# Kernel optimization log

Measured on AMD Instinct MI355X. Metric: run time of the kernel, lower is better.

Reference implementation:

```python
import jax, jax.numpy as jnp
import numpy as np

EPS = 1e-5  # torch BatchNorm2d default eps

def _bn_train(x, g, b):
    # BatchNorm2d in training mode: batch statistics over (N, H, W), biased variance
    m = x.mean(axis=(0, 2, 3), keepdims=True)
    v = x.var(axis=(0, 2, 3), keepdims=True)
    return g[None, :, None, None] * (x - m) / jnp.sqrt(v + EPS) + b[None, :, None, None]

def _conv3(x, w, b):
    y = jax.lax.conv_general_dilated(x, w, (1, 1), 'SAME',
                                     dimension_numbers=('NCHW', 'OIHW', 'NCHW'))
    return y + b[None, :, None, None]

def _conv1(x, w, b):
    # 1x1 conv == per-pixel matmul; w: [out, in]
    return jnp.einsum('bchw,oc->bohw', x, w) + b[None, :, None, None]

def _projector(x, w1, b1, g1, be1, w2, b2, g2, be2):
    h = jax.nn.relu(_bn_train(_conv3(x, w1, b1), g1, be1))
    return _bn_train(_conv1(h, w2, b2), g2, be2)

def _cross_teacher_attention(s, teachers, wq, bq, wk, bk, wv, bv):
    B, C, H, W = s.shape
    scale = C ** -0.5
    q = _conv1(s, wq, bq).reshape(B, C, H * W).transpose(0, 2, 1)  # [B, HW, C]
    outs, ws = [], []
    for t in teachers:  # small fixed list of teachers (structural branch)
        k = _conv1(t, wk, bk).reshape(B, C, H * W).transpose(0, 2, 1)
        v = _conv1(t, wv, bv).reshape(B, C, H * W).transpose(0, 2, 1)
        a = jax.nn.softmax(jnp.einsum('bqc,bkc->bqk', q, k) * scale, axis=-1)  # [B, HW, HW]
        outs.append(jnp.einsum('bqk,bkc->bqc', a, v))                          # [B, HW, C]
        ws.append(a.mean(axis=-1))                                             # [B, HW]
    w = jax.nn.softmax(jnp.stack(ws, axis=-1), axis=-1)          # [B, HW, T]
    fused = jnp.einsum('bqt,tbqc->bqc', w, jnp.stack(outs, 0))   # weighted sum over teachers
    fused = fused.reshape(B, H, W, C).transpose(0, 3, 1, 2)      # [B, C, H, W]
    return s + fused

def setup_inputs() -> dict:
    key = jax.random.key(0)
    ks = jax.random.split(key, 16)
    B, C, H, W = 8, 128, 56, 56
    T = 256  # teacher projector output dim
    d = {}
    d['student_mid'] = jax.random.normal(ks[0], (B, C, H, W), jnp.float32)
    d['t1_mid'] = jax.random.normal(ks[1], (B, C, H, W), jnp.float32)
    d['t2_mid'] = jax.random.normal(ks[2], (B, C, H, W), jnp.float32)
    for i, n in enumerate(['q', 'k', 'v']):
        d['w' + n] = jax.random.normal(ks[3 + i], (C, C), jnp.float32) * 0.05
        d['b' + n] = jnp.zeros((C,), jnp.float32)
    for p, off in (('p1', 6), ('p2', 10)):
        d[p + '_w1'] = jax.random.normal(ks[off], (C, C, 3, 3), jnp.float32) * 0.05
        d[p + '_b1'] = jnp.zeros((C,), jnp.float32)
        d[p + '_g1'] = jnp.ones((C,), jnp.float32)
        d[p + '_be1'] = jnp.zeros((C,), jnp.float32)
        d[p + '_w2'] = jax.random.normal(ks[off + 1], (T, C), jnp.float32) * 0.05
        d[p + '_b2'] = jnp.zeros((T,), jnp.float32)
        d[p + '_g2'] = jnp.ones((T,), jnp.float32)
        d[p + '_be2'] = jnp.zeros((T,), jnp.float32)
    return d

def reference(student_mid, t1_mid, t2_mid, wq, bq, wk, bk, wv, bv,
              p1_w1, p1_b1, p1_g1, p1_be1, p1_w2, p1_b2, p1_g2, p1_be2,
              p2_w1, p2_b1, p2_g1, p2_be1, p2_w2, p2_b2, p2_g2, p2_be2):
    # Per-teacher projectors: computed by the torch module but their outputs are
    # never consumed by the attention (s_feat_proj is unused) -> dead code.
    _sp1 = _projector(student_mid, p1_w1, p1_b1, p1_g1, p1_be1, p1_w2, p1_b2, p1_g2, p1_be2)
    _sp2 = _projector(student_mid, p2_w1, p2_b1, p2_g1, p2_be1, p2_w2, p2_b2, p2_g2, p2_be2)
    del _sp1, _sp2
    return _cross_teacher_attention(student_mid, [t1_mid, t2_mid], wq, bq, wk, bk, wv, bv)
```

## Files before the change

### kernel.cpp

```cpp
#include <hip/hip_runtime.h>

#define HW 3136
#define NB 8
#define CD 128
#define QSCALE 0.12751750206f

typedef __attribute__((ext_vector_type(8))) short short8;
typedef __attribute__((ext_vector_type(4))) float floatx4;
typedef __attribute__((ext_vector_type(4))) unsigned short ushort4v;

static __device__ __forceinline__ unsigned short f2b(float f){
  union { float f; unsigned u; } v; v.f = f;
  unsigned r = v.u + 0x7FFFu + ((v.u >> 16) & 1u);
  return (unsigned short)(r >> 16);
}
static __device__ __forceinline__ float b2f(unsigned short h){
  union { unsigned u; float f; } v; v.u = ((unsigned)h) << 16;
  return v.f;
}

__global__ __launch_bounds__(256) void proj_kernel(
    const float* __restrict__ s, const float* __restrict__ t1, const float* __restrict__ t2,
    const float* __restrict__ wq, const float* __restrict__ bq,
    const float* __restrict__ wk, const float* __restrict__ bk,
    const float* __restrict__ wv, const float* __restrict__ bv,
    unsigned short* __restrict__ qkv)
{
  __shared__ __align__(16) unsigned short WL[CD][136];
  __shared__ __align__(16) unsigned short xsT[64][136];
  const int job = blockIdx.z;
  const float* x; const float* w; const float* bias; float scl; int cmajor; size_t dstoff;
  switch(job){
    case 0: x=s;  w=wq; bias=bq; scl=QSCALE; cmajor=0; dstoff=0; break;
    case 1: x=t1; w=wk; bias=bk; scl=1.f;    cmajor=0; dstoff=1; break;
    case 2: x=t1; w=wv; bias=bv; scl=1.f;    cmajor=1; dstoff=2; break;
    case 3: x=t2; w=wk; bias=bk; scl=1.f;    cmajor=0; dstoff=3; break;
    default:x=t2; w=wv; bias=bv; scl=1.f;    cmajor=1; dstoff=4; break;
  }
  const size_t TS = (size_t)NB*HW*CD;
  const int b   = blockIdx.y;
  const int hw0 = blockIdx.x * 64;
  const int tid = threadIdx.x;

  for (int i = 0; i < 16; i++){
    int flat = tid + i*256;
    int o = flat >> 5, cq = (flat & 31)*4;
    floatx4 wv4 = *(const floatx4*)(w + (size_t)o*CD + cq);
    ushort4v pk;
    for (int j=0;j<4;j++) pk[j] = f2b(wv4[j]);
    *(ushort4v*)&WL[o][cq] = pk;
  }
  const float* xb = x + (size_t)b*CD*HW + hw0;
  for (int i = 0; i < 8; i++){
    int flat = (tid + i*256)*4;
    int c = flat >> 6, hh = flat & 63;
    floatx4 xv = *(const floatx4*)(xb + (size_t)c*HW + hh);
    for (int j=0;j<4;j++) xsT[hh+j][c] = f2b(xv[j]);
  }
  __syncthreads();

  const int m = tid & 15, quad = (tid >> 4) & 3, wv_ = tid >> 6;
  short8 af[4];
  for (int dk=0;dk<4;dk++)
    af[dk] = *(const short8*)&xsT[wv_*16 + m][dk*32 + quad*8];
  float bb[8];
  for (int nt=0;nt<8;nt++) bb[nt] = bias[nt*16 + m];

  unsigned short* dstK = qkv + dstoff*TS + ((size_t)b*HW + hw0)*CD;
  unsigned short* dstV = qkv + dstoff*TS + (size_t)b*CD*HW;
  for (int nt=0;nt<8;nt++){
    floatx4 acc = {bb[nt],bb[nt],bb[nt],bb[nt]};
    for (int dk=0;dk<4;dk++){
      short8 bf = *(const short8*)&WL[nt*16 + m][dk*32 + quad*8];
      acc = __builtin_amdgcn_mfma_f32_16x16x32_bf16(af[dk], bf, acc, 0,0,0);
    }
    if (!cmajor){
      for (int r=0;r<4;r++)
        dstK[(size_t)(wv_*16 + quad*4 + r)*CD + nt*16 + m] = f2b(acc[r]*scl);
    } else {
      ushort4v pk;
      for (int r=0;r<4;r++) pk[r] = f2b(acc[r]*scl);
      *(ushort4v*)&dstV[(size_t)(nt*16 + m)*HW + hw0 + wv_*16 + quad*4] = pk;
    }
  }
}

#define KL_E (64*136)
#define VL_E (128*72)
#define PL_E (4*16*72)

__global__ __launch_bounds__(256,3) void attn_kernel(
    const unsigned short* __restrict__ qkv,
    unsigned short* __restrict__ Og)
{
  __shared__ __align__(16) unsigned short smem[KL_E + VL_E + PL_E];
  unsigned short (*Kl)[136] = (unsigned short(*)[136])smem;
  unsigned short (*Vl)[72]  = (unsigned short(*)[72])(smem + KL_E);
  unsigned short (*Pl)[72]  = (unsigned short(*)[72])(smem + KL_E + VL_E);

  const int qt = blockIdx.x;
  const int b  = blockIdx.y;
  const int t  = blockIdx.z;
  const size_t TS = (size_t)NB*HW*CD;
  const unsigned short* Q = qkv + (size_t)b*HW*CD;
  const unsigned short* K = qkv + TS*(size_t)(1 + 2*t) + (size_t)b*HW*CD;
  const unsigned short* V = qkv + TS*(size_t)(2 + 2*t) + (size_t)b*CD*HW;

  const int tid  = threadIdx.x;
  const int wv_  = tid >> 6;
  const int lane = tid & 63;
  const int m    = lane & 15;
  const int quad = lane >> 4;
  const int q0   = qt*64 + wv_*16;

  short8 qf[4];
  {
    const unsigned short* qr = Q + (size_t)(q0+m)*CD + quad*8;
    for (int dk=0;dk<4;dk++) qf[dk] = *(const short8*)(qr + dk*32);
  }
  floatx4 Oc[8];
  for (int i=0;i<8;i++) Oc[i] = (floatx4)0.f;
  float lr[4] = {0.f,0.f,0.f,0.f};

  const unsigned short* kg = K + (size_t)(tid>>4)*CD + (tid&15)*8;
  const unsigned short* vg = V + (size_t)(tid>>3)*HW + (tid&7)*8;
  unsigned short* klds = &Kl[tid>>4][(tid&15)*8];
  unsigned short* vlds = &Vl[tid>>3][(tid&7)*8];

  short8 kpre[4], vpre[4];
  for (int i=0;i<4;i++) kpre[i] = *(const short8*)(kg + (size_t)i*16*CD);
  for (int i=0;i<4;i++) vpre[i] = *(const short8*)(vg + (size_t)i*32*HW);

  for (int kt = 0; kt < HW/64; kt++){
    __syncthreads();
    for (int i=0;i<4;i++) *(short8*)(klds + i*16*136) = kpre[i];
    for (int i=0;i<4;i++) *(short8*)(vlds + i*32*72)  = vpre[i];
    __syncthreads();
    if (kt < HW/64 - 1){
      kg += 64*CD; vg += 64;
      for (int i=0;i<4;i++) kpre[i] = *(const short8*)(kg + (size_t)i*16*CD);
      for (int i=0;i<4;i++) vpre[i] = *(const short8*)(vg + (size_t)i*32*HW);
    }

    floatx4 sc[4];
    for (int nt=0;nt<4;nt++){
      floatx4 acc = (floatx4)0.f;
      for (int dk=0;dk<4;dk++){
        short8 kf = *(const short8*)&Kl[nt*16 + m][dk*32 + quad*8];
        acc = __builtin_amdgcn_mfma_f32_16x16x32_bf16(qf[dk], kf, acc, 0,0,0);
      }
      sc[nt] = acc;
    }
    for (int nt=0;nt<4;nt++){
      for (int r=0;r<4;r++){
        float p = __builtin_amdgcn_exp2f(sc[nt][r]);
        lr[r] += p;
        union { float f; unsigned u; } cv; cv.f = p;
        Pl[wv_*16 + quad*4 + r][nt*16 + m] = (unsigned short)(cv.u >> 16);
      }
    }
    __asm__ volatile("s_waitcnt lgkmcnt(0)" ::: "memory");
    for (int ct=0;ct<8;ct++){
      floatx4 o = Oc[ct];
      for (int kk=0;kk<2;kk++){
        short8 pf = *(const short8*)&Pl[wv_*16 + m][kk*32 + quad*8];
        short8 vf = *(const short8*)&Vl[ct*16 + m][kk*32 + quad*8];
        o = __builtin_amdgcn_mfma_f32_16x16x32_bf16(pf, vf, o, 0,0,0);
      }
      Oc[ct] = o;
    }
  }

  for (int r=0;r<4;r++)
    for (int off=1; off<16; off<<=1)
      lr[r] += __shfl_xor(lr[r], off, 64);
  float inv[4];
  for (int r=0;r<4;r++) inv[r] = 1.f / lr[r];

  __syncthreads();
  float* stg = ((float*)smem) + wv_*(16*132);
  for (int ct=0;ct<8;ct++)
    for (int r=0;r<4;r++)
      stg[(quad*4+r)*132 + ct*16 + m] = Oc[ct][r]*inv[r];
  __syncthreads();
  unsigned short* ob = Og + ((size_t)t*NB + b)*HW*CD + (size_t)q0*CD;
  for (int row=0; row<16; row++){
    float v0 = stg[row*132 + 2*lane];
    float v1 = stg[row*132 + 2*lane + 1];
    unsigned short pk[2] = {f2b(v0), f2b(v1)};
    *(unsigned int*)&ob[(size_t)row*CD + 2*lane] = *(const unsigned int*)pk;
  }
}

__global__ __launch_bounds__(256) void combine_kernel(
    const float* __restrict__ s, const unsigned short* __restrict__ Og,
    float* __restrict__ out)
{
  __shared__ float T[32][129];
  const int b   = blockIdx.y;
  const int hw0 = blockIdx.x * 32;
  const int tid = threadIdx.x;
  const unsigned short* O1 = Og + ((size_t)b*HW + hw0)*CD;
  const unsigned short* O2 = O1 + (size_t)NB*HW*CD;
  for (int i=0;i<2;i++){
    int flat = (tid + i*256)*8;
    int row = flat >> 7, col = flat & 127;
    short8 a  = *(const short8*)(O1 + (size_t)row*CD + col);
    short8 c2 = *(const short8*)(O2 + (size_t)row*CD + col);
    for (int j=0;j<8;j++)
      T[row][col+j] = 0.5f*(b2f((unsigned short)a[j]) + b2f((unsigned short)c2[j]));
  }
  __syncthreads();
  const int c  = tid >> 1;
  const int h0 = (tid & 1)*16;
  const float* sr = s   + ((size_t)b*CD + c)*HW + hw0 + h0;
  float*     orow = out + ((size_t)b*CD + c)*HW + hw0 + h0;
  for (int j0=0;j0<16;j0+=4){
    floatx4 sv = *(const floatx4*)(sr + j0);
    floatx4 ov;
    for (int jj=0;jj<4;jj++) ov[jj] = sv[jj] + T[h0+j0+jj][c];
    *(floatx4*)(orow + j0) = ov;
  }
}

extern "C" void kernel_launch(void* const* d_in, const int* in_sizes, int n_in,
                              void* d_out, int out_size, void* d_ws, size_t ws_size,
                              hipStream_t stream)
{
  const float* s  = (const float*)d_in[0];
  const float* t1 = (const float*)d_in[1];
  const float* t2 = (const float*)d_in[2];
  const float* wq = (const float*)d_in[3];
  const float* bq = (const float*)d_in[4];
  const float* wk = (const float*)d_in[5];
  const float* bk = (const float*)d_in[6];
  const float* wv = (const float*)d_in[7];
  const float* bv = (const float*)d_in[8];
  float* out = (float*)d_out;

  unsigned short* qkv = (unsigned short*)d_ws;
  unsigned short* Og  = qkv + (size_t)5*NB*HW*CD;

  hipLaunchKernelGGL(proj_kernel,    dim3(49,8,5), dim3(256), 0, stream,
                     s,t1,t2,wq,bq,wk,bk,wv,bv,qkv);
  hipLaunchKernelGGL(attn_kernel,    dim3(49,8,2), dim3(256), 0, stream, qkv, Og);
  hipLaunchKernelGGL(combine_kernel, dim3(98,8),   dim3(256), 0, stream, s, Og, out);
}
```

Baseline: 307.1 us.

## Keep attention probabilities in registers via transposed MFMA and lane shuffles

The attention kernel swaps the MFMA operand order so the score and output tiles come out transposed, then repacks the bf16 probabilities in registers with cross-lane shuffles. This replaces the round-trip through the shared-memory P buffer. With that buffer gone, LDS use per block drops and the launch-bounds occupancy hint rises from 3 to 4. The cost is extra shuffle instructions and selects per tile, and register pressure at the higher occupancy target could cause spills.

```diff
diff --git a/kernel.cpp b/kernel.cpp
--- a/kernel.cpp
+++ b/kernel.cpp
@@ -87,16 +87,14 @@
 
 #define KL_E (64*136)
 #define VL_E (128*72)
-#define PL_E (4*16*72)
-
-__global__ __launch_bounds__(256,3) void attn_kernel(
+
+__global__ __launch_bounds__(256,4) void attn_kernel(
     const unsigned short* __restrict__ qkv,
     unsigned short* __restrict__ Og)
 {
-  __shared__ __align__(16) unsigned short smem[KL_E + VL_E + PL_E];
+  __shared__ __align__(16) unsigned short smem[KL_E + VL_E];
   unsigned short (*Kl)[136] = (unsigned short(*)[136])smem;
   unsigned short (*Vl)[72]  = (unsigned short(*)[72])(smem + KL_E);
-  unsigned short (*Pl)[72]  = (unsigned short(*)[72])(smem + KL_E + VL_E);
 
   const int qt = blockIdx.x;
   const int b  = blockIdx.y;
@@ -120,7 +118,7 @@
   }
   floatx4 Oc[8];
   for (int i=0;i<8;i++) Oc[i] = (floatx4)0.f;
-  float lr[4] = {0.f,0.f,0.f,0.f};
+  float lr = 0.f;
 
   const unsigned short* kg = K + (size_t)(tid>>4)*CD + (tid&15)*8;
   const unsigned short* vg = V + (size_t)(tid>>3)*HW + (tid&7)*8;
@@ -130,6 +128,10 @@
   short8 kpre[4], vpre[4];
   for (int i=0;i<4;i++) kpre[i] = *(const short8*)(kg + (size_t)i*16*CD);
   for (int i=0;i<4;i++) vpre[i] = *(const short8*)(vg + (size_t)i*32*HW);
+
+  const int sl0 = (((quad<<1)    ) & 3)*16 + m;
+  const int sl1 = (((quad<<1) + 1) & 3)*16 + m;
+  const bool hiq = (quad >= 2);
 
   for (int kt = 0; kt < HW/64; kt++){
     __syncthreads();
@@ -142,46 +144,56 @@
       for (int i=0;i<4;i++) vpre[i] = *(const short8*)(vg + (size_t)i*32*HW);
     }
 
-    floatx4 sc[4];
+    unsigned pw[8];
     for (int nt=0;nt<4;nt++){
       floatx4 acc = (floatx4)0.f;
       for (int dk=0;dk<4;dk++){
         short8 kf = *(const short8*)&Kl[nt*16 + m][dk*32 + quad*8];
-        acc = __builtin_amdgcn_mfma_f32_16x16x32_bf16(qf[dk], kf, acc, 0,0,0);
+        acc = __builtin_amdgcn_mfma_f32_16x16x32_bf16(kf, qf[dk], acc, 0,0,0);
       }
-      sc[nt] = acc;
-    }
-    for (int nt=0;nt<4;nt++){
-      for (int r=0;r<4;r++){
-        float p = __builtin_amdgcn_exp2f(sc[nt][r]);
-        lr[r] += p;
-        union { float f; unsigned u; } cv; cv.f = p;
-        Pl[wv_*16 + quad*4 + r][nt*16 + m] = (unsigned short)(cv.u >> 16);
+      union { float f; unsigned u; } c0, c1, c2, c3;
+      c0.f = __builtin_amdgcn_exp2f(acc[0]);
+      c1.f = __builtin_amdgcn_exp2f(acc[1]);
+      c2.f = __builtin_amdgcn_exp2f(acc[2]);
+      c3.f = __builtin_amdgcn_exp2f(acc[3]);
+      lr += (c0.f + c1.f) + (c2.f + c3.f);
+      pw[nt*2+0] = (c1.u & 0xFFFF0000u) | (c0.u >> 16);
+      pw[nt*2+1] = (c3.u & 0xFFFF0000u) | (c2.u >> 16);
+    }
+
+    short8 pf[2];
+    for (int kk=0;kk<2;kk++){
+      union { unsigned u[4]; short8 s; } bf_;
+      for (int w=0;w<4;w++){
+        int sl = (w>>1) ? sl1 : sl0;
+        int lo = __shfl((int)pw[4*kk     + (w&1)], sl, 64);
+        int hi = __shfl((int)pw[4*kk + 2 + (w&1)], sl, 64);
+        bf_.u[w] = hiq ? (unsigned)hi : (unsigned)lo;
       }
-    }
-    __asm__ volatile("s_waitcnt lgkmcnt(0)" ::: "memory");
+      pf[kk] = bf_.s;
+    }
+
     for (int ct=0;ct<8;ct++){
       floatx4 o = Oc[ct];
       for (int kk=0;kk<2;kk++){
-        short8 pf = *(const short8*)&Pl[wv_*16 + m][kk*32 + quad*8];
         short8 vf = *(const short8*)&Vl[ct*16 + m][kk*32 + quad*8];
-        o = __builtin_amdgcn_mfma_f32_16x16x32_bf16(pf, vf, o, 0,0,0);
+        o = __builtin_amdgcn_mfma_f32_16x16x32_bf16(vf, pf[kk], o, 0,0,0);
       }
       Oc[ct] = o;
     }
   }
 
-  for (int r=0;r<4;r++)
-    for (int off=1; off<16; off<<=1)
-      lr[r] += __shfl_xor(lr[r], off, 64);
-  float inv[4];
-  for (int r=0;r<4;r++) inv[r] = 1.f / lr[r];
+  lr += __shfl_xor(lr, 16, 64);
+  lr += __shfl_xor(lr, 32, 64);
+  const float inv = 1.f / lr;
 
   __syncthreads();
   float* stg = ((float*)smem) + wv_*(16*132);
-  for (int ct=0;ct<8;ct++)
-    for (int r=0;r<4;r++)
-      stg[(quad*4+r)*132 + ct*16 + m] = Oc[ct][r]*inv[r];
+  for (int ct=0;ct<8;ct++){
+    floatx4 vv;
+    for (int r=0;r<4;r++) vv[r] = Oc[ct][r]*inv;
+    *(floatx4*)&stg[m*132 + ct*16 + quad*4] = vv;
+  }
   __syncthreads();
   unsigned short* ob = Og + ((size_t)t*NB + b)*HW*CD + (size_t)q0*CD;
   for (int row=0; row<16; row++){
```

Result: slower. 313.7 us (+2.1%).
